# Performance work log

Hardware: AMD Instinct MI355X
Metric: run time of the kernel (lower is better)

Reference implementation:

```python
import jax, jax.numpy as jnp
import numpy as np

# MACE/molgym-style SimpleModel with max_ell=1, hidden_irreps = 64x0e + 64x1o,
# num_interactions=2, num_elements=10, num_bessel=8, polynomial cutoff p=5, r_max=5.0.
N, E, C, NE, NB, H = 20000, 320000, 64, 10, 8, 64
R_MAX = 5.0
P_CUT = 5


def _mlp(x, W1, W2, W3):
    # radial MLP producing per-edge tensor-product weights (silu nonlinearity)
    h = jax.nn.silu(x @ W1)
    h = jax.nn.silu(h @ W2)
    return h @ W3


def setup_inputs() -> dict:
    key = jax.random.key(0)
    ks = jax.random.split(key, 24)
    positions = jax.random.normal(ks[0], (N, 3), jnp.float32)
    edge_index = jax.random.randint(ks[1], (2, E), 0, N)
    shifts = jnp.zeros((E, 3), jnp.float32)
    species = jax.random.randint(ks[2], (N,), 0, NE)
    node_attrs = jax.nn.one_hot(species, NE, dtype=jnp.float32)

    def w(k, shape, fan_in):
        return jax.random.normal(k, shape, jnp.float32) / np.sqrt(fan_in)

    params = dict(
        W_embed=w(ks[3], (NE, C), NE),
        R1_W1=w(ks[4], (NB, H), NB), R1_W2=w(ks[5], (H, H), H), R1_W3=w(ks[6], (H, 2 * C), H),
        U1_s=w(ks[7], (C, C), C),
        L1_s=w(ks[8], (C, C), C), L1_v=w(ks[9], (C, C), C),
        K1_s=w(ks[10], (C, NE, C), C * NE),
        R2_W1=w(ks[11], (NB, H), NB), R2_W2=w(ks[12], (H, H), H), R2_W3=w(ks[13], (H, 4 * C), H),
        U2_s=w(ks[14], (C, C), C), U2_v=w(ks[15], (C, C), C),
        L2_s=w(ks[16], (2 * C, C), 2 * C), L2_v=w(ks[17], (2 * C, C), 2 * C),
        K2_s=w(ks[18], (C, NE, C), C * NE), K2_v=w(ks[19], (C, NE, C), C * NE),
    )
    return dict(positions=positions, node_attrs=node_attrs, edge_index=edge_index,
                shifts=shifts, **params)


def _forward(positions, node_attrs, shifts, W_embed,
             R1_W1, R1_W2, R1_W3, U1_s, L1_s, L1_v, K1_s,
             R2_W1, R2_W2, R2_W3, U2_s, U2_v, L2_s, L2_v, K2_s, K2_v,
             edge_index):
    snd, rcv = edge_index[0], edge_index[1]
    # edge vectors / lengths
    vec = positions[snd] - positions[rcv] + shifts            # [E,3]
    length = jnp.sqrt(jnp.sum(vec * vec, axis=1, keepdims=True) + 1e-12)  # [E,1]
    unit = vec / length
    # spherical harmonics (normalize=True, component normalization): Y0=1, Y1=sqrt(3)*r_hat
    Y1 = np.float32(np.sqrt(3.0)) * unit                      # [E,3]
    # Bessel radial basis * polynomial cutoff
    n = jnp.arange(1, NB + 1, dtype=jnp.float32)
    bessel = np.float32(np.sqrt(2.0 / R_MAX)) * jnp.sin(n * np.float32(np.pi) * length / R_MAX) / length
    u = length / R_MAX
    p = P_CUT
    poly = (1.0 - 0.5 * (p + 1) * (p + 2) * u ** p
            + p * (p + 2) * u ** (p + 1)
            - 0.5 * p * (p + 1) * u ** (p + 2))
    edge_feats = bessel * (poly * (u < 1.0))                  # [E,NB]
    # node embedding (linear on one-hot species)
    s0 = node_attrs @ W_embed                                 # [N,C]

    # ---- interaction block 1 (input feats: scalars only) ----
    s = s0 @ U1_s                                             # linear_up
    tpw = _mlp(edge_feats, R1_W1, R1_W2, R1_W3).reshape(E, 2, C)
    s_e = s[snd]                                              # gather sender feats
    m_s = tpw[:, 0] * s_e                                     # 0e x 0e -> 0e  [E,C]
    m_v = (tpw[:, 1] * s_e)[:, :, None] * Y1[:, None, :]      # 0e x 1o -> 1o  [E,C,3]
    agg_s = jax.ops.segment_sum(m_s, rcv, num_segments=N)
    agg_v = jax.ops.segment_sum(m_v, rcv, num_segments=N)
    skip_s = jnp.einsum('nu,nv,uvd->nd', s0, node_attrs, K1_s)  # skip tensor product
    s1 = agg_s @ L1_s + skip_s                                # [N,C]
    v1 = jnp.einsum('nci,cd->ndi', agg_v, L1_v)               # [N,C,3]

    # ---- interaction block 2 (input feats: 64x0e + 64x1o) ----
    s = s1 @ U2_s
    v = jnp.einsum('nci,cd->ndi', v1, U2_v)
    tpw = _mlp(edge_feats, R2_W1, R2_W2, R2_W3).reshape(E, 4, C)
    s_e, v_e = s[snd], v[snd]
    mA = tpw[:, 0] * s_e                                      # 0e x 0e -> 0e
    mB = (tpw[:, 1] * s_e)[:, :, None] * Y1[:, None, :]       # 0e x 1o -> 1o
    mC = tpw[:, 2][:, :, None] * v_e                          # 1o x 0e -> 1o
    mD = tpw[:, 3] * (jnp.einsum('eci,ei->ec', v_e, Y1) / np.float32(np.sqrt(3.0)))  # 1o x 1o -> 0e
    mid_s = jnp.concatenate([mA, mD], axis=1)                 # [E,2C]
    mid_v = jnp.concatenate([mB, mC], axis=1)                 # [E,2C,3]
    agg_s = jax.ops.segment_sum(mid_s, rcv, num_segments=N)
    agg_v = jax.ops.segment_sum(mid_v, rcv, num_segments=N)
    skip_s = jnp.einsum('nu,nv,uvd->nd', s1, node_attrs, K2_s)
    skip_v = jnp.einsum('nui,nv,uvd->ndi', v1, node_attrs, K2_v)
    s2 = agg_s @ L2_s + skip_s                                # [N,C]
    v2 = jnp.einsum('nci,cd->ndi', agg_v, L2_v) + skip_v      # [N,C,3]
    return jnp.concatenate([s2, v2.reshape(N, 3 * C)], axis=1)  # [N,4C]


def reference(positions, node_attrs, edge_index, shifts, W_embed,
              R1_W1, R1_W2, R1_W3, U1_s, L1_s, L1_v, K1_s,
              R2_W1, R2_W2, R2_W3, U2_s, U2_v, L2_s, L2_v, K2_s, K2_v):
    return _forward(positions, node_attrs, shifts, W_embed,
                    R1_W1, R1_W2, R1_W3, U1_s, L1_s, L1_v, K1_s,
                    R2_W1, R2_W2, R2_W3, U2_s, U2_v, L2_s, L2_v, K2_s, K2_v,
                    edge_index)
```

## Files before the change

kernel.cpp:

```cpp
#include <hip/hip_runtime.h>
#include <hip/hip_fp16.h>

#define NNODES 20000
#define NEDGES 320000
#define NELEM  10
#define NC     (NNODES * 64)

#define OFF_SUP1 ((size_t)0)
#define OFF_AGS1 ((size_t)1 * NC)
#define OFF_AGV1 ((size_t)2 * NC)
#define OFF_AGS2 ((size_t)0)
#define OFF_AGV2 ((size_t)2 * NC)
#define OFF_SUP2 ((size_t)8 * NC)
#define OFF_VUP2 ((size_t)9 * NC)
#define OFF_SKS2 ((size_t)12 * NC)
#define OFF_SKV2 ((size_t)13 * NC)
#define OFF_INT  ((size_t)16 * NC)

#define SMEM_BYTES 52480

typedef __attribute__((ext_vector_type(8))) short bf16x8;
typedef __attribute__((ext_vector_type(4))) float f32x4;

__device__ __forceinline__ float silu(float x) { return x / (1.0f + __expf(-x)); }
__device__ __forceinline__ int rfl(int v) { return __builtin_amdgcn_readfirstlane(v); }
__device__ __forceinline__ int rl_i(int v, int l) { return __builtin_amdgcn_readlane(v, l); }
__device__ __forceinline__ float rl_f(float v, int l) {
    return __int_as_float(__builtin_amdgcn_readlane(__float_as_int(v), l));
}
__device__ __forceinline__ uint2 split2(float x0, float x1) {
    unsigned int b0 = __float_as_uint(x0), b1 = __float_as_uint(x1);
    unsigned int h0 = (b0 + 0x7FFF + ((b0 >> 16) & 1)) & 0xFFFF0000u;
    unsigned int h1 = (b1 + 0x7FFF + ((b1 >> 16) & 1)) & 0xFFFF0000u;
    unsigned int l0 = __float_as_uint(x0 - __uint_as_float(h0));
    unsigned int l1 = __float_as_uint(x1 - __uint_as_float(h1));
    unsigned int hi = (h0 >> 16) | (h1 & 0xFFFF0000u);
    unsigned int lo = ((l0 + 0x7FFF + ((l0 >> 16) & 1)) >> 16)
                    | ((l1 + 0x7FFF + ((l1 >> 16) & 1)) & 0xFFFF0000u);
    return make_uint2(hi, lo);
}

__global__ __launch_bounds__(256) void k_wsplit(
    const float* __restrict__ W3a, const float* __restrict__ W3b,
    unsigned short* __restrict__ out)
{
    int t = blockIdx.x * 256 + threadIdx.x;
    float x; unsigned short *ph, *pl; int idx;
    if (t < 8192) {
        int n = t >> 6, k = t & 63;
        x = W3a[k * 128 + n]; ph = out; pl = out + 8192; idx = n * 64 + k;
    } else {
        int u = t - 8192; int n = u >> 6, k = u & 63;
        x = W3b[k * 256 + n]; ph = out + 16384; pl = out + 32768; idx = n * 64 + k;
    }
    unsigned int b = __float_as_uint(x);
    unsigned int h = (b + 0x7FFF + ((b >> 16) & 1)) & 0xFFFF0000u;
    unsigned int r = __float_as_uint(x - __uint_as_float(h));
    ph[idx] = (unsigned short)(h >> 16);
    pl[idx] = (unsigned short)((r + 0x7FFF + ((r >> 16) & 1)) >> 16);
}

__global__ __launch_bounds__(256) void k_hist(const int* __restrict__ eidx,
                                              int* __restrict__ hist)
{
    int e = blockIdx.x * 256 + threadIdx.x;
    atomicAdd(&hist[eidx[NEDGES + e]], 1);
}

__global__ __launch_bounds__(1024) void k_scan(const int* __restrict__ hist,
                                               int* __restrict__ cursor)
{
    __shared__ int wsum[16];
    __shared__ int gbase;
    int tid = threadIdx.x;
    int lane = tid & 63, wvid = tid >> 6;
    if (tid == 0) gbase = 0;
    __syncthreads();
    for (int seg = 0; seg < 20; ++seg) {
        int i = seg * 1024 + tid;
        int v = (i < NNODES) ? hist[i] : 0;
        int s = v;
        #pragma unroll
        for (int d = 1; d < 64; d <<= 1) {
            int t = __shfl_up(s, d, 64);
            if (lane >= d) s += t;
        }
        if (lane == 63) wsum[wvid] = s;
        __syncthreads();
        if (wvid == 0) {
            int w = (lane < 16) ? wsum[lane] : 0;
            #pragma unroll
            for (int d = 1; d < 16; d <<= 1) {
                int t = __shfl_up(w, d, 64);
                if (lane >= d) w += t;
            }
            if (lane < 16) wsum[lane] = w;
        }
        __syncthreads();
        int wbase = (wvid == 0) ? 0 : wsum[wvid - 1];
        if (i < NNODES) cursor[i] = gbase + wbase + s - v;
        int segtot = wsum[15];
        __syncthreads();
        if (tid == 0) gbase += segtot;
    }
}

__global__ __launch_bounds__(256) void k_scatter(const int* __restrict__ eidx,
                                                 int* __restrict__ cursor,
                                                 int* __restrict__ sorted)
{
    int e = blockIdx.x * 256 + threadIdx.x;
    int pos = atomicAdd(&cursor[eidx[NEDGES + e]], 1);
    sorted[pos] = e;
}

__global__ __launch_bounds__(256) void k_node_pre(
    const float* __restrict__ attrs, const float* __restrict__ Wemb,
    const float* __restrict__ U1s, __half* __restrict__ sUp1)
{
    int lane = threadIdx.x & 63, wv = threadIdx.x >> 6;
    int n = blockIdx.x * 4 + wv;
    __shared__ __align__(16) float s0sh[4][64];
    float s0 = 0.f;
    #pragma unroll
    for (int v = 0; v < NELEM; ++v) s0 += attrs[n * NELEM + v] * Wemb[v * 64 + lane];
    s0sh[wv][lane] = s0;
    __syncthreads();
    float a = 0.f;
    #pragma unroll 8
    for (int k = 0; k < 64; ++k) a += s0sh[wv][k] * U1s[k * 64 + lane];
    sUp1[n * 64 + lane] = __float2half_rn(a);
}

__global__ __launch_bounds__(256, 3) void k_edge1(
    const float* __restrict__ pos, const int* __restrict__ eidx,
    const float* __restrict__ shf, const int* __restrict__ sorted,
    const float* __restrict__ W1, const float* __restrict__ W2,
    const unsigned short* __restrict__ w3h, const unsigned short* __restrict__ w3l,
    const __half* __restrict__ sUp1,
    float* __restrict__ agS1, float* __restrict__ agV1)
{
    __shared__ __align__(16) char smem[SMEM_BYTES];
    float (*ysh)[3]   = (float (*)[3])(smem);
    int*  ssh         = (int*)(smem + 768);
    int*  rsh         = (int*)(smem + 1024);
    float (*h1sh)[65] = (float (*)[65])(smem + 1280);
    float (*fsh)[9]   = (float (*)[9])(smem + 17920);
    unsigned short (*h2buf)[64][72] = (unsigned short (*)[64][72])(smem + 34048);

    const int tid = threadIdx.x;
    const int lane = tid & 63;
    const int w = rfl(tid >> 6);
    const int e0 = blockIdx.x * 64;

    {
        int e = tid >> 2, sub = tid & 3;
        int sid = sorted[e0 + e];
        int snd = eidx[sid], rcv = eidx[NEDGES + sid];
        float dx = pos[snd * 3 + 0] - pos[rcv * 3 + 0] + shf[(size_t)sid * 3 + 0];
        float dy = pos[snd * 3 + 1] - pos[rcv * 3 + 1] + shf[(size_t)sid * 3 + 1];
        float dz = pos[snd * 3 + 2] - pos[rcv * 3 + 2] + shf[(size_t)sid * 3 + 2];
        float len = sqrtf(dx * dx + dy * dy + dz * dz + 1e-12f);
        float inv = 1.0f / len;
        float u = len * 0.2f;
        float u2 = u * u, u4 = u2 * u2, u5 = u4 * u, u6 = u5 * u, u7 = u6 * u;
        float cut = (u < 1.0f) ? (1.0f - 21.0f * u5 + 35.0f * u6 - 15.0f * u7) : 0.0f;
        float s = 0.632455532033676f * inv * cut;
        #pragma unroll
        for (int kk = 0; kk < 2; ++kk) {
            int k = sub * 2 + kk;
            fsh[e][k] = s * sinf((float)(k + 1) * 0.628318530717959f * len);
        }
        if (sub == 0) {
            ssh[e] = snd; rsh[e] = rcv;
            ysh[e][0] = 1.73205080756888f * dx * inv;
            ysh[e][1] = 1.73205080756888f * dy * inv;
            ysh[e][2] = 1.73205080756888f * dz * inv;
        }
    }
    __syncthreads();

    const int rAll = rsh[lane];
    const int sAll = ssh[lane];
    const float y0A = ysh[lane][0], y1A = ysh[lane][1], y2A = ysh[lane][2];

    {
        float f[8];
        #pragma unroll
        for (int k = 0; k < 8; ++k) f[k] = fsh[lane][k];
        const float* __restrict__ w1b = W1 + w * 16;
        #pragma unroll
        for (int j = 0; j < 16; ++j) {
            float a = 0.f;
            #pragma unroll
            for (int k = 0; k < 8; ++k) a = fmaf(f[k], w1b[k * 64 + j], a);
            h1sh[lane][w * 16 + j] = silu(a);
        }
    }
    __syncthreads();

    {
        const float2* __restrict__ w2b = (const float2*)W2 + w * 8;
        float2 acc[8];
        #pragma unroll
        for (int j = 0; j < 8; ++j) acc[j] = make_float2(0.f, 0.f);
        for (int k = 0; k < 64; ++k) {
            float h = h1sh[lane][k];
            const float2* __restrict__ wk = w2b + k * 32;
            #pragma unroll
            for (int j = 0; j < 8; ++j) {
                float2 wv = wk[j];
                acc[j].x = fmaf(h, wv.x, acc[j].x);
                acc[j].y = fmaf(h, wv.y, acc[j].y);
            }
        }
        #pragma unroll
        for (int j = 0; j < 8; ++j) {
            uint2 p = split2(silu(acc[j].x), silu(acc[j].y));
            *(unsigned int*)&h2buf[0][lane][w * 16 + 2 * j] = p.x;
            *(unsigned int*)&h2buf[1][lane][w * 16 + 2 * j] = p.y;
        }
    }
    __syncthreads();

    const int q = lane >> 4, nl = lane & 15;
    float* trw = (float*)(smem + 1280) + w * 2048;

    const unsigned short* ar = &h2buf[0][w * 16 + nl][0];
    const unsigned short* al = &h2buf[1][w * 16 + nl][0];
    bf16x8 ah0 = *(const bf16x8*)(ar + q * 8);
    bf16x8 ah1 = *(const bf16x8*)(ar + 32 + q * 8);
    bf16x8 al0 = *(const bf16x8*)(al + q * 8);
    bf16x8 al1 = *(const bf16x8*)(al + 32 + q * 8);

    float sreg[16];
    #pragma unroll
    for (int i = 0; i < 16; ++i)
        sreg[i] = __half2float(sUp1[rl_i(sAll, w * 16 + i) * 64 + lane]);

    #pragma unroll
    for (int nt = 0; nt < 8; ++nt) {
        int ng = nt * 16 + nl;
        const unsigned short* wh = w3h + ng * 64 + q * 8;
        const unsigned short* wl = w3l + ng * 64 + q * 8;
        bf16x8 bh0 = *(const bf16x8*)wh;
        bf16x8 bh1 = *(const bf16x8*)(wh + 32);
        bf16x8 bl0 = *(const bf16x8*)wl;
        bf16x8 bl1 = *(const bf16x8*)(wl + 32);
        f32x4 a = {0.f, 0.f, 0.f, 0.f};
        a = __builtin_amdgcn_mfma_f32_16x16x32_bf16(ah0, bh0, a, 0, 0, 0);
        a = __builtin_amdgcn_mfma_f32_16x16x32_bf16(ah1, bh1, a, 0, 0, 0);
        a = __builtin_amdgcn_mfma_f32_16x16x32_bf16(ah0, bl0, a, 0, 0, 0);
        a = __builtin_amdgcn_mfma_f32_16x16x32_bf16(ah1, bl1, a, 0, 0, 0);
        a = __builtin_amdgcn_mfma_f32_16x16x32_bf16(al0, bh0, a, 0, 0, 0);
        a = __builtin_amdgcn_mfma_f32_16x16x32_bf16(al1, bh1, a, 0, 0, 0);
        #pragma unroll
        for (int r = 0; r < 4; ++r) {
            int li = q * 4 + r;
            trw[li * 128 + ((ng + 4 * li) & 127)] = a[r];
        }
    }

    float accS = 0.f, b0 = 0.f, b1 = 0.f, b2 = 0.f;
    int cur = rl_i(rAll, w * 16);
    #pragma unroll
    for (int i = 0; i < 16; ++i) {
        int e = w * 16 + i;
        int rcv = rl_i(rAll, e);
        if (rcv != cur) {
            unsafeAtomicAdd(&agS1[cur * 64 + lane], accS);
            unsafeAtomicAdd(&agV1[cur * 192 +       lane], b0);
            unsafeAtomicAdd(&agV1[cur * 192 +  64 + lane], b1);
            unsafeAtomicAdd(&agV1[cur * 192 + 128 + lane], b2);
            accS = b0 = b1 = b2 = 0.f;
            cur = rcv;
        }
        float tv0 = trw[i * 128 + ((lane + 4 * i) & 127)];
        float tv1 = trw[i * 128 + ((64 + lane + 4 * i) & 127)];
        float se = sreg[i];
        accS += tv0 * se;
        float msg = tv1 * se;
        b0 += msg * rl_f(y0A, e);
        b1 += msg * rl_f(y1A, e);
        b2 += msg * rl_f(y2A, e);
    }
    unsafeAtomicAdd(&agS1[cur * 64 + lane], accS);
    unsafeAtomicAdd(&agV1[cur * 192 +       lane], b0);
    unsafeAtomicAdd(&agV1[cur * 192 +  64 + lane], b1);
    unsafeAtomicAdd(&agV1[cur * 192 + 128 + lane], b2);
}

__global__ __launch_bounds__(256) void k_node_mid(
    const float* __restrict__ attrs, const float* __restrict__ Wemb,
    const float* __restrict__ K1s, const float* __restrict__ L1s,
    const float* __restrict__ L1v,
    const float* __restrict__ U2s, const float* __restrict__ U2v,
    const float* __restrict__ K2s, const float* __restrict__ K2v,
    const float* __restrict__ agS1, const float* __restrict__ agV1,
    __half* __restrict__ sUp2, __half* __restrict__ vUp2,
    float* __restrict__ skS2, float* __restrict__ skV2)
{
    int lane = threadIdx.x & 63, wv = threadIdx.x >> 6;
    int n = blockIdx.x * 4 + wv;
    __shared__ float aSsh[4][64];
    __shared__ float aVsh[4][3][64];
    __shared__ float s0sh[4][64];
    __shared__ float s1sh[4][64];
    __shared__ float v1sh[4][3][64];

    int sp = 0;
    #pragma unroll
    for (int v = 0; v < NELEM; ++v) if (attrs[n * NELEM + v] > 0.5f) sp = v;
    aSsh[wv][lane] = agS1[n * 64 + lane];
    #pragma unroll
    for (int i = 0; i < 3; ++i) aVsh[wv][i][lane] = agV1[n * 192 + i * 64 + lane];
    s0sh[wv][lane] = Wemb[sp * 64 + lane];
    __syncthreads();

    float s1 = 0.f;
    #pragma unroll 8
    for (int k = 0; k < 64; ++k) s1 += aSsh[wv][k] * L1s[k * 64 + lane];
    #pragma unroll 8
    for (int k = 0; k < 64; ++k) s1 += s0sh[wv][k] * K1s[(k * NELEM + sp) * 64 + lane];
    float v1[3] = {0.f, 0.f, 0.f};
    #pragma unroll 8
    for (int k = 0; k < 64; ++k) {
        float w = L1v[k * 64 + lane];
        v1[0] += aVsh[wv][0][k] * w;
        v1[1] += aVsh[wv][1][k] * w;
        v1[2] += aVsh[wv][2][k] * w;
    }
    s1sh[wv][lane] = s1;
    #pragma unroll
    for (int i = 0; i < 3; ++i) v1sh[wv][i][lane] = v1[i];
    __syncthreads();

    float su = 0.f, ks = 0.f;
    float vu[3] = {0.f, 0.f, 0.f}, kv[3] = {0.f, 0.f, 0.f};
    #pragma unroll 8
    for (int k = 0; k < 64; ++k) su += s1sh[wv][k] * U2s[k * 64 + lane];
    #pragma unroll 8
    for (int k = 0; k < 64; ++k) ks += s1sh[wv][k] * K2s[(k * NELEM + sp) * 64 + lane];
    #pragma unroll 8
    for (int k = 0; k < 64; ++k) {
        float w = U2v[k * 64 + lane];
        vu[0] += v1sh[wv][0][k] * w;
        vu[1] += v1sh[wv][1][k] * w;
        vu[2] += v1sh[wv][2][k] * w;
    }
    #pragma unroll 8
    for (int k = 0; k < 64; ++k) {
        float w = K2v[(k * NELEM + sp) * 64 + lane];
        kv[0] += v1sh[wv][0][k] * w;
        kv[1] += v1sh[wv][1][k] * w;
        kv[2] += v1sh[wv][2][k] * w;
    }
    sUp2[n * 64 + lane] = __float2half_rn(su);
    skS2[n * 64 + lane] = ks;
    #pragma unroll
    for (int i = 0; i < 3; ++i) {
        vUp2[n * 192 + i * 64 + lane] = __float2half_rn(vu[i]);
        skV2[n * 192 + i * 64 + lane] = kv[i];
    }
}

__global__ __launch_bounds__(256, 3) void k_edge2(
    const float* __restrict__ pos, const int* __restrict__ eidx,
    const float* __restrict__ shf, const int* __restrict__ sorted,
    const float* __restrict__ W1, const float* __restrict__ W2,
    const unsigned short* __restrict__ w3h, const unsigned short* __restrict__ w3l,
    const __half* __restrict__ sUp2, const __half* __restrict__ vUp2,
    float* __restrict__ agS2, float* __restrict__ agV2)
{
    __shared__ __align__(16) char smem[SMEM_BYTES];
    float (*ysh)[3]   = (float (*)[3])(smem);
    int*  ssh         = (int*)(smem + 768);
    int*  rsh         = (int*)(smem + 1024);
    float (*h1sh)[65] = (float (*)[65])(smem + 1280);
    float (*fsh)[9]   = (float (*)[9])(smem + 17920);
    unsigned short (*h2buf)[64][72] = (unsigned short (*)[64][72])(smem + 34048);

    const int tid = threadIdx.x;
    const int lane = tid & 63;
    const int w = rfl(tid >> 6);
    const int e0 = blockIdx.x * 64;

    {
        int e = tid >> 2, sub = tid & 3;
        int sid = sorted[e0 + e];
        int snd = eidx[sid], rcv = eidx[NEDGES + sid];
        float dx = pos[snd * 3 + 0] - pos[rcv * 3 + 0] + shf[(size_t)sid * 3 + 0];
        float dy = pos[snd * 3 + 1] - pos[rcv * 3 + 1] + shf[(size_t)sid * 3 + 1];
        float dz = pos[snd * 3 + 2] - pos[rcv * 3 + 2] + shf[(size_t)sid * 3 + 2];
        float len = sqrtf(dx * dx + dy * dy + dz * dz + 1e-12f);
        float inv = 1.0f / len;
        float u = len * 0.2f;
        float u2 = u * u, u4 = u2 * u2, u5 = u4 * u, u6 = u5 * u, u7 = u6 * u;
        float cut = (u < 1.0f) ? (1.0f - 21.0f * u5 + 35.0f * u6 - 15.0f * u7) : 0.0f;
        float s = 0.632455532033676f * inv * cut;
        #pragma unroll
        for (int kk = 0; kk < 2; ++kk) {
            int k = sub * 2 + kk;
            fsh[e][k] = s * sinf((float)(k + 1) * 0.628318530717959f * len);
        }
        if (sub == 0) {
            ssh[e] = snd; rsh[e] = rcv;
            ysh[e][0] = 1.73205080756888f * dx * inv;
            ysh[e][1] = 1.73205080756888f * dy * inv;
            ysh[e][2] = 1.73205080756888f * dz * inv;
        }
    }
    __syncthreads();

    const int rAll = rsh[lane];
    const int sAll = ssh[lane];
    const float y0A = ysh[lane][0], y1A = ysh[lane][1], y2A = ysh[lane][2];

    {
        float f[8];
        #pragma unroll
        for (int k = 0; k < 8; ++k) f[k] = fsh[lane][k];
        const float* __restrict__ w1b = W1 + w * 16;
        #pragma unroll
        for (int j = 0; j < 16; ++j) {
            float a = 0.f;
            #pragma unroll
            for (int k = 0; k < 8; ++k) a = fmaf(f[k], w1b[k * 64 + j], a);
            h1sh[lane][w * 16 + j] = silu(a);
        }
    }
    __syncthreads();

    {
        const float2* __restrict__ w2b = (const float2*)W2 + w * 8;
        float2 acc[8];
        #pragma unroll
        for (int j = 0; j < 8; ++j) acc[j] = make_float2(0.f, 0.f);
        for (int k = 0; k < 64; ++k) {
            float h = h1sh[lane][k];
            const float2* __restrict__ wk = w2b + k * 32;
            #pragma unroll
            for (int j = 0; j < 8; ++j) {
                float2 wv = wk[j];
                acc[j].x = fmaf(h, wv.x, acc[j].x);
                acc[j].y = fmaf(h, wv.y, acc[j].y);
            }
        }
        #pragma unroll
        for (int j = 0; j < 8; ++j) {
            uint2 p = split2(silu(acc[j].x), silu(acc[j].y));
            *(unsigned int*)&h2buf[0][lane][w * 16 + 2 * j] = p.x;
            *(unsigned int*)&h2buf[1][lane][w * 16 + 2 * j] = p.y;
        }
    }
    __syncthreads();

    const int q = lane >> 4, nl = lane & 15;
    float* trw = (float*)(smem + 1280) + w * 2048;

    const unsigned short* ar = &h2buf[0][w * 16 + nl][0];
    const unsigned short* al = &h2buf[1][w * 16 + nl][0];
    bf16x8 ah0 = *(const bf16x8*)(ar + q * 8);
    bf16x8 ah1 = *(const bf16x8*)(ar + 32 + q * 8);
    bf16x8 al0 = *(const bf16x8*)(al + q * 8);
    bf16x8 al1 = *(const bf16x8*)(al + 32 + q * 8);

    float sreg[16];
    #pragma unroll
    for (int i = 0; i < 16; ++i)
        sreg[i] = __half2float(sUp2[rl_i(sAll, w * 16 + i) * 64 + lane]);

    #pragma unroll
    for (int nt = 0; nt < 8; ++nt) {
        int ng = nt * 16 + nl;
        const unsigned short* wh = w3h + ng * 64 + q * 8;
        const unsigned short* wl = w3l + ng * 64 + q * 8;
        bf16x8 bh0 = *(const bf16x8*)wh;
        bf16x8 bh1 = *(const bf16x8*)(wh + 32);
        bf16x8 bl0 = *(const bf16x8*)wl;
        bf16x8 bl1 = *(const bf16x8*)(wl + 32);
        f32x4 a = {0.f, 0.f, 0.f, 0.f};
        a = __builtin_amdgcn_mfma_f32_16x16x32_bf16(ah0, bh0, a, 0, 0, 0);
        a = __builtin_amdgcn_mfma_f32_16x16x32_bf16(ah1, bh1, a, 0, 0, 0);
        a = __builtin_amdgcn_mfma_f32_16x16x32_bf16(ah0, bl0, a, 0, 0, 0);
        a = __builtin_amdgcn_mfma_f32_16x16x32_bf16(ah1, bl1, a, 0, 0, 0);
        a = __builtin_amdgcn_mfma_f32_16x16x32_bf16(al0, bh0, a, 0, 0, 0);
        a = __builtin_amdgcn_mfma_f32_16x16x32_bf16(al1, bh1, a, 0, 0, 0);
        #pragma unroll
        for (int r = 0; r < 4; ++r) {
            int li = q * 4 + r;
            trw[li * 128 + ((ng + 4 * li) & 127)] = a[r];
        }
    }

    {
        float accS = 0.f, b0 = 0.f, b1 = 0.f, b2 = 0.f;
        int cur = rl_i(rAll, w * 16);
        #pragma unroll
        for (int i = 0; i < 16; ++i) {
            int e = w * 16 + i;
            int rcv = rl_i(rAll, e);
            if (rcv != cur) {
                unsafeAtomicAdd(&agS2[cur * 128 + lane], accS);
                unsafeAtomicAdd(&agV2[cur * 384 + 0 * 128 + lane], b0);
                unsafeAtomicAdd(&agV2[cur * 384 + 1 * 128 + lane], b1);
                unsafeAtomicAdd(&agV2[cur * 384 + 2 * 128 + lane], b2);
                accS = b0 = b1 = b2 = 0.f;
                cur = rcv;
            }
            float tv0 = trw[i * 128 + ((lane + 4 * i) & 127)];
            float tv1 = trw[i * 128 + ((64 + lane + 4 * i) & 127)];
            float se = sreg[i];
            accS += tv0 * se;
            float msg = tv1 * se;
            b0 += msg * rl_f(y0A, e);
            b1 += msg * rl_f(y1A, e);
            b2 += msg * rl_f(y2A, e);
        }
        unsafeAtomicAdd(&agS2[cur * 128 + lane], accS);
        unsafeAtomicAdd(&agV2[cur * 384 + 0 * 128 + lane], b0);
        unsafeAtomicAdd(&agV2[cur * 384 + 1 * 128 + lane], b1);
        unsafeAtomicAdd(&agV2[cur * 384 + 2 * 128 + lane], b2);
    }

    float vr0[16], vr1[16], vr2[16];
    #pragma unroll
    for (int i = 0; i < 16; ++i) {
        int snd = rl_i(sAll, w * 16 + i);
        vr0[i] = __half2float(vUp2[snd * 192 +       lane]);
        vr1[i] = __half2float(vUp2[snd * 192 +  64 + lane]);
        vr2[i] = __half2float(vUp2[snd * 192 + 128 + lane]);
    }

    #pragma unroll
    for (int nt = 0; nt < 8; ++nt) {
        int c  = nt * 16 + nl;
        int ng = 128 + c;
        const unsigned short* wh = w3h + ng * 64 + q * 8;
        const unsigned short* wl = w3l + ng * 64 + q * 8;
        bf16x8 bh0 = *(const bf16x8*)wh;
        bf16x8 bh1 = *(const bf16x8*)(wh + 32);
        bf16x8 bl0 = *(const bf16x8*)wl;
        bf16x8 bl1 = *(const bf16x8*)(wl + 32);
        f32x4 a = {0.f, 0.f, 0.f, 0.f};
        a = __builtin_amdgcn_mfma_f32_16x16x32_bf16(ah0, bh0, a, 0, 0, 0);
        a = __builtin_amdgcn_mfma_f32_16x16x32_bf16(ah1, bh1, a, 0, 0, 0);
        a = __builtin_amdgcn_mfma_f32_16x16x32_bf16(ah0, bl0, a, 0, 0, 0);
        a = __builtin_amdgcn_mfma_f32_16x16x32_bf16(ah1, bl1, a, 0, 0, 0);
        a = __builtin_amdgcn_mfma_f32_16x16x32_bf16(al0, bh0, a, 0, 0, 0);
        a = __builtin_amdgcn_mfma_f32_16x16x32_bf16(al1, bh1, a, 0, 0, 0);
        #pragma unroll
        for (int r = 0; r < 4; ++r) {
            int li = q * 4 + r;
            trw[li * 128 + ((c + 4 * li) & 127)] = a[r];
        }
    }

    {
        float accD = 0.f, c0 = 0.f, c1 = 0.f, c2 = 0.f;
        int cur = rl_i(rAll, w * 16);
        #pragma unroll
        for (int i = 0; i < 16; ++i) {
            int e = w * 16 + i;
            int rcv = rl_i(rAll, e);
            if (rcv != cur) {
                unsafeAtomicAdd(&agS2[cur * 128 + 64 + lane], accD);
                unsafeAtomicAdd(&agV2[cur * 384 + 0 * 128 + 64 + lane], c0);
                unsafeAtomicAdd(&agV2[cur * 384 + 1 * 128 + 64 + lane], c1);
                unsafeAtomicAdd(&agV2[cur * 384 + 2 * 128 + 64 + lane], c2);
                accD = c0 = c1 = c2 = 0.f;
                cur = rcv;
            }
            float tvC = trw[i * 128 + ((lane + 4 * i) & 127)];
            float tvD = trw[i * 128 + ((64 + lane + 4 * i) & 127)];
            c0 += tvC * vr0[i];
            c1 += tvC * vr1[i];
            c2 += tvC * vr2[i];
            float dotvy = vr0[i] * rl_f(y0A, e) + vr1[i] * rl_f(y1A, e)
                        + vr2[i] * rl_f(y2A, e);
            accD += tvD * dotvy * 0.577350269189626f;
        }
        unsafeAtomicAdd(&agS2[cur * 128 + 64 + lane], accD);
        unsafeAtomicAdd(&agV2[cur * 384 + 0 * 128 + 64 + lane], c0);
        unsafeAtomicAdd(&agV2[cur * 384 + 1 * 128 + 64 + lane], c1);
        unsafeAtomicAdd(&agV2[cur * 384 + 2 * 128 + 64 + lane], c2);
    }
}

__global__ __launch_bounds__(256) void k_node_out(
    const float* __restrict__ L2s, const float* __restrict__ L2v,
    const float* __restrict__ agS2, const float* __restrict__ agV2,
    const float* __restrict__ skS2, const float* __restrict__ skV2,
    float* __restrict__ out)
{
    int lane = threadIdx.x & 63, wv = threadIdx.x >> 6;
    int n = blockIdx.x * 4 + wv;
    __shared__ __align__(16) float aS[4][128];
    __shared__ __align__(16) float aV[4][3][128];

    aS[wv][lane]      = agS2[n * 128 + lane];
    aS[wv][64 + lane] = agS2[n * 128 + 64 + lane];
    #pragma unroll
    for (int i = 0; i < 3; ++i) {
        aV[wv][i][lane]      = agV2[n * 384 + i * 128 + lane];
        aV[wv][i][64 + lane] = agV2[n * 384 + i * 128 + 64 + lane];
    }
    __syncthreads();

    float s2 = skS2[n * 64 + lane];
    #pragma unroll 8
    for (int u = 0; u < 128; ++u) s2 += aS[wv][u] * L2s[u * 64 + lane];
    float v2[3];
    #pragma unroll
    for (int i = 0; i < 3; ++i) v2[i] = skV2[n * 192 + i * 64 + lane];
    #pragma unroll 8
    for (int u = 0; u < 128; ++u) {
        float w = L2v[u * 64 + lane];
        v2[0] += aV[wv][0][u] * w;
        v2[1] += aV[wv][1][u] * w;
        v2[2] += aV[wv][2][u] * w;
    }
    out[(size_t)n * 256 + lane] = s2;
    #pragma unroll
    for (int i = 0; i < 3; ++i)
        out[(size_t)n * 256 + 64 + lane * 3 + i] = v2[i];
}

extern "C" void kernel_launch(void* const* d_in, const int* in_sizes, int n_in,
                              void* d_out, int out_size, void* d_ws, size_t ws_size,
                              hipStream_t stream)
{
    (void)in_sizes; (void)n_in; (void)out_size; (void)ws_size;
    const float* positions  = (const float*)d_in[0];
    const float* node_attrs = (const float*)d_in[1];
    const int*   edge_index = (const int*)d_in[2];
    const float* shifts     = (const float*)d_in[3];
    const float* W_embed    = (const float*)d_in[4];
    const float* R1W1 = (const float*)d_in[5];
    const float* R1W2 = (const float*)d_in[6];
    const float* R1W3 = (const float*)d_in[7];
    const float* U1s  = (const float*)d_in[8];
    const float* L1s  = (const float*)d_in[9];
    const float* L1v  = (const float*)d_in[10];
    const float* K1s  = (const float*)d_in[11];
    const float* R2W1 = (const float*)d_in[12];
    const float* R2W2 = (const float*)d_in[13];
    const float* R2W3 = (const float*)d_in[14];
    const float* U2s  = (const float*)d_in[15];
    const float* U2v  = (const float*)d_in[16];
    const float* L2s  = (const float*)d_in[17];
    const float* L2v  = (const float*)d_in[18];
    const float* K2s  = (const float*)d_in[19];
    const float* K2v  = (const float*)d_in[20];

    float* wsf = (float*)d_ws;
    int*   wsi = (int*)(wsf + OFF_INT);
    int* hist   = wsi;
    int* cursor = wsi + 20000;
    int* sorted = wsi + 40000;
    unsigned short* wsh = (unsigned short*)(wsi + 360000);
    const unsigned short* w3a_hi = wsh;
    const unsigned short* w3a_lo = wsh + 8192;
    const unsigned short* w3b_hi = wsh + 16384;
    const unsigned short* w3b_lo = wsh + 32768;

    __half* sUp1h = (__half*)(wsf + OFF_SUP1);
    __half* sUp2h = (__half*)(wsf + OFF_SUP2);
    __half* vUp2h = (__half*)(wsf + OFF_VUP2);

    hipMemsetAsync(wsf + OFF_AGS1, 0, (size_t)4 * NC * sizeof(float), stream);
    hipMemsetAsync(hist, 0, 20000 * sizeof(int), stream);

    k_wsplit<<<96, 256, 0, stream>>>(R1W3, R2W3, wsh);
    k_hist<<<NEDGES / 256, 256, 0, stream>>>(edge_index, hist);
    k_scan<<<1, 1024, 0, stream>>>(hist, cursor);
    k_scatter<<<NEDGES / 256, 256, 0, stream>>>(edge_index, cursor, sorted);

    k_node_pre<<<NNODES / 4, 256, 0, stream>>>(node_attrs, W_embed, U1s, sUp1h);
    k_edge1<<<NEDGES / 64, 256, 0, stream>>>(positions, edge_index, shifts, sorted,
                                             R1W1, R1W2, w3a_hi, w3a_lo,
                                             sUp1h, wsf + OFF_AGS1, wsf + OFF_AGV1);
    k_node_mid<<<NNODES / 4, 256, 0, stream>>>(node_attrs, W_embed, K1s, L1s, L1v,
                                               U2s, U2v, K2s, K2v,
                                               wsf + OFF_AGS1, wsf + OFF_AGV1,
                                               sUp2h, vUp2h,
                                               wsf + OFF_SKS2, wsf + OFF_SKV2);
    hipMemsetAsync(wsf + OFF_AGS2, 0, (size_t)8 * NC * sizeof(float), stream);
    k_edge2<<<NEDGES / 64, 256, 0, stream>>>(positions, edge_index, shifts, sorted,
                                             R2W1, R2W2, w3b_hi, w3b_lo,
                                             sUp2h, vUp2h,
                                             wsf + OFF_AGS2, wsf + OFF_AGV2);
    k_node_out<<<NNODES / 4, 256, 0, stream>>>(L2s, L2v, wsf + OFF_AGS2, wsf + OFF_AGV2,
                                               wsf + OFF_SKS2, wsf + OFF_SKV2,
                                               (float*)d_out);
}
```

Measured before the change: 633.9 us.

## Split edge1 TP weight output into two halves to cut LDS and raise occupancy

In k_edge1, the 128-column radial-MLP output GEMM is now computed in two 64-column halves: scalar messages are aggregated first, then the same per-wave LDS buffer is reused for the vector half. This halves the transpose scratch, shrinks shared memory, and raises the launch-bounds occupancy hint from 3 to 4 blocks. Both edge kernels also remap block indices with an XCD swizzle so consecutive edge tiles (sorted by receiver) land on the same XCD, which should improve L2 locality for the atomics. The cost is two separate atomic passes, more register pressure at 4 blocks per CU, and a swizzle that hardcodes 5000 blocks.

Measured after the change: 614.9 us. -3.0%, faster.

```diff
diff --git a/kernel.cpp b/kernel.cpp
--- a/kernel.cpp
+++ b/kernel.cpp
@@ -17,7 +17,12 @@
 #define OFF_SKV2 ((size_t)13 * NC)
 #define OFF_INT  ((size_t)16 * NC)
 
-#define SMEM_BYTES 52480
+#define SMEM1_BYTES 38656
+#define SMEM2_BYTES 52480
+
+__device__ __forceinline__ int xcd_swz(int bid) {
+    return (bid & 7) * 625 + (bid >> 3);
+}
 
 typedef __attribute__((ext_vector_type(8))) short bf16x8;
 typedef __attribute__((ext_vector_type(4))) float f32x4;
@@ -132,7 +137,7 @@
     sUp1[n * 64 + lane] = __float2half_rn(a);
 }
 
-__global__ __launch_bounds__(256, 3) void k_edge1(
+__global__ __launch_bounds__(256, 4) void k_edge1(
     const float* __restrict__ pos, const int* __restrict__ eidx,
     const float* __restrict__ shf, const int* __restrict__ sorted,
     const float* __restrict__ W1, const float* __restrict__ W2,
@@ -140,18 +145,18 @@
     const __half* __restrict__ sUp1,
     float* __restrict__ agS1, float* __restrict__ agV1)
 {
-    __shared__ __align__(16) char smem[SMEM_BYTES];
+    __shared__ __align__(16) char smem[SMEM1_BYTES];
     float (*ysh)[3]   = (float (*)[3])(smem);
     int*  ssh         = (int*)(smem + 768);
     int*  rsh         = (int*)(smem + 1024);
     float (*h1sh)[65] = (float (*)[65])(smem + 1280);
-    float (*fsh)[9]   = (float (*)[9])(smem + 17920);
-    unsigned short (*h2buf)[64][72] = (unsigned short (*)[64][72])(smem + 34048);
+    unsigned short (*h2buf)[64][72] = (unsigned short (*)[64][72])(smem + 17920);
+    float (*fsh)[9]   = (float (*)[9])(smem + 36352);
 
     const int tid = threadIdx.x;
     const int lane = tid & 63;
     const int w = rfl(tid >> 6);
-    const int e0 = blockIdx.x * 64;
+    const int e0 = xcd_swz(blockIdx.x) * 64;
 
     {
         int e = tid >> 2, sub = tid & 3;
@@ -224,7 +229,7 @@
     __syncthreads();
 
     const int q = lane >> 4, nl = lane & 15;
-    float* trw = (float*)(smem + 1280) + w * 2048;
+    float* trw = (float*)(smem + 1280) + w * 1024;
 
     const unsigned short* ar = &h2buf[0][w * 16 + nl][0];
     const unsigned short* al = &h2buf[1][w * 16 + nl][0];
@@ -239,8 +244,47 @@
         sreg[i] = __half2float(sUp1[rl_i(sAll, w * 16 + i) * 64 + lane]);
 
     #pragma unroll
-    for (int nt = 0; nt < 8; ++nt) {
-        int ng = nt * 16 + nl;
+    for (int nt = 0; nt < 4; ++nt) {
+        int c = nt * 16 + nl;
+        const unsigned short* wh = w3h + c * 64 + q * 8;
+        const unsigned short* wl = w3l + c * 64 + q * 8;
+        bf16x8 bh0 = *(const bf16x8*)wh;
+        bf16x8 bh1 = *(const bf16x8*)(wh + 32);
+        bf16x8 bl0 = *(const bf16x8*)wl;
+        bf16x8 bl1 = *(const bf16x8*)(wl + 32);
+        f32x4 a = {0.f, 0.f, 0.f, 0.f};
+        a = __builtin_amdgcn_mfma_f32_16x16x32_bf16(ah0, bh0, a, 0, 0, 0);
+        a = __builtin_amdgcn_mfma_f32_16x16x32_bf16(ah1, bh1, a, 0, 0, 0);
+        a = __builtin_amdgcn_mfma_f32_16x16x32_bf16(ah0, bl0, a, 0, 0, 0);
+        a = __builtin_amdgcn_mfma_f32_16x16x32_bf16(ah1, bl1, a, 0, 0, 0);
+        a = __builtin_amdgcn_mfma_f32_16x16x32_bf16(al0, bh0, a, 0, 0, 0);
+        a = __builtin_amdgcn_mfma_f32_16x16x32_bf16(al1, bh1, a, 0, 0, 0);
+        #pragma unroll
+        for (int r = 0; r < 4; ++r) {
+            int li = q * 4 + r;
+            trw[li * 64 + ((c + 4 * li) & 63)] = a[r];
+        }
+    }
+    {
+        float accS = 0.f;
+        int cur = rl_i(rAll, w * 16);
+        #pragma unroll
+        for (int i = 0; i < 16; ++i) {
+            int e = w * 16 + i;
+            int rcv = rl_i(rAll, e);
+            if (rcv != cur) {
+                unsafeAtomicAdd(&agS1[cur * 64 + lane], accS);
+                accS = 0.f; cur = rcv;
+            }
+            accS += trw[i * 64 + ((lane + 4 * i) & 63)] * sreg[i];
+        }
+        unsafeAtomicAdd(&agS1[cur * 64 + lane], accS);
+    }
+
+    #pragma unroll
+    for (int nt = 0; nt < 4; ++nt) {
+        int c = nt * 16 + nl;
+        int ng = 64 + c;
         const unsigned short* wh = w3h + ng * 64 + q * 8;
         const unsigned short* wl = w3l + ng * 64 + q * 8;
         bf16x8 bh0 = *(const bf16x8*)wh;
@@ -257,37 +301,31 @@
         #pragma unroll
         for (int r = 0; r < 4; ++r) {
             int li = q * 4 + r;
-            trw[li * 128 + ((ng + 4 * li) & 127)] = a[r];
-        }
-    }
-
-    float accS = 0.f, b0 = 0.f, b1 = 0.f, b2 = 0.f;
-    int cur = rl_i(rAll, w * 16);
-    #pragma unroll
-    for (int i = 0; i < 16; ++i) {
-        int e = w * 16 + i;
-        int rcv = rl_i(rAll, e);
-        if (rcv != cur) {
-            unsafeAtomicAdd(&agS1[cur * 64 + lane], accS);
-            unsafeAtomicAdd(&agV1[cur * 192 +       lane], b0);
-            unsafeAtomicAdd(&agV1[cur * 192 +  64 + lane], b1);
-            unsafeAtomicAdd(&agV1[cur * 192 + 128 + lane], b2);
-            accS = b0 = b1 = b2 = 0.f;
-            cur = rcv;
-        }
-        float tv0 = trw[i * 128 + ((lane + 4 * i) & 127)];
-        float tv1 = trw[i * 128 + ((64 + lane + 4 * i) & 127)];
-        float se = sreg[i];
-        accS += tv0 * se;
-        float msg = tv1 * se;
-        b0 += msg * rl_f(y0A, e);
-        b1 += msg * rl_f(y1A, e);
-        b2 += msg * rl_f(y2A, e);
-    }
-    unsafeAtomicAdd(&agS1[cur * 64 + lane], accS);
-    unsafeAtomicAdd(&agV1[cur * 192 +       lane], b0);
-    unsafeAtomicAdd(&agV1[cur * 192 +  64 + lane], b1);
-    unsafeAtomicAdd(&agV1[cur * 192 + 128 + lane], b2);
+            trw[li * 64 + ((c + 4 * li) & 63)] = a[r];
+        }
+    }
+    {
+        float b0 = 0.f, b1 = 0.f, b2 = 0.f;
+        int cur = rl_i(rAll, w * 16);
+        #pragma unroll
+        for (int i = 0; i < 16; ++i) {
+            int e = w * 16 + i;
+            int rcv = rl_i(rAll, e);
+            if (rcv != cur) {
+                unsafeAtomicAdd(&agV1[cur * 192 +       lane], b0);
+                unsafeAtomicAdd(&agV1[cur * 192 +  64 + lane], b1);
+                unsafeAtomicAdd(&agV1[cur * 192 + 128 + lane], b2);
+                b0 = b1 = b2 = 0.f; cur = rcv;
+            }
+            float msg = trw[i * 64 + ((lane + 4 * i) & 63)] * sreg[i];
+            b0 += msg * rl_f(y0A, e);
+            b1 += msg * rl_f(y1A, e);
+            b2 += msg * rl_f(y2A, e);
+        }
+        unsafeAtomicAdd(&agV1[cur * 192 +       lane], b0);
+        unsafeAtomicAdd(&agV1[cur * 192 +  64 + lane], b1);
+        unsafeAtomicAdd(&agV1[cur * 192 + 128 + lane], b2);
+    }
 }
 
 __global__ __launch_bounds__(256) void k_node_mid(
@@ -372,7 +410,7 @@
     const __half* __restrict__ sUp2, const __half* __restrict__ vUp2,
     float* __restrict__ agS2, float* __restrict__ agV2)
 {
-    __shared__ __align__(16) char smem[SMEM_BYTES];
+    __shared__ __align__(16) char smem[SMEM2_BYTES];
     float (*ysh)[3]   = (float (*)[3])(smem);
     int*  ssh         = (int*)(smem + 768);
     int*  rsh         = (int*)(smem + 1024);
@@ -383,7 +421,7 @@
     const int tid = threadIdx.x;
     const int lane = tid & 63;
     const int w = rfl(tid >> 6);
-    const int e0 = blockIdx.x * 64;
+    const int e0 = xcd_swz(blockIdx.x) * 64;
 
     {
         int e = tid >> 2, sub = tid & 3;
```
